# Performance work log

Measured on AMD Instinct MI355X. Metric: run time of the kernel, lower is better.

Reference implementation:

```python
import jax, jax.numpy as jnp
import numpy as np

D_MODEL = 1024
N_HEAD = 16
D_HEAD = D_MODEL // N_HEAD


def setup_inputs() -> dict:
    key = jax.random.key(0)
    ks = jax.random.split(key, 5)
    x = jax.random.normal(ks[0], (4, 2048, D_MODEL), dtype=jnp.float32)
    s = 1.0 / np.sqrt(D_MODEL)
    W_qkv = jax.random.normal(ks[1], (D_MODEL, 3 * D_MODEL), dtype=jnp.float32) * s
    b_qkv = jnp.zeros((3 * D_MODEL,), dtype=jnp.float32)
    W_out = jax.random.normal(ks[2], (D_MODEL, D_MODEL), dtype=jnp.float32) * s
    b_out = jnp.zeros((D_MODEL,), dtype=jnp.float32)
    return {"x": x, "W_qkv": W_qkv, "b_qkv": b_qkv, "W_out": W_out, "b_out": b_out}


def reference(x, W_qkv, b_qkv, W_out, b_out):
    B, T, C = x.shape
    qkv = x @ W_qkv + b_qkv                      # [B,T,3C]
    q, k, v = jnp.split(qkv, 3, axis=-1)
    def heads(t):
        return t.reshape(B, T, N_HEAD, D_HEAD).transpose(0, 2, 1, 3)  # [B,H,T,Dh]
    q, k, v = heads(q), heads(k), heads(v)
    scale = 1.0 / np.sqrt(D_HEAD)
    attn = jnp.einsum('bhqd,bhkd->bhqk', q, k) * scale  # [B,H,T,T]
    causal = jnp.tril(jnp.ones((T, T), dtype=bool))
    attn = jnp.where(causal, attn, -jnp.inf)
    attn = jax.nn.softmax(attn, axis=-1)
    out = jnp.einsum('bhqk,bhkd->bhqd', attn, v)  # [B,H,T,Dh]
    out = out.transpose(0, 2, 1, 3).reshape(B, T, C)
    return out @ W_out + b_out
```

## Files before the change

### kernel.cpp

```cpp
#include <hip/hip_runtime.h>

typedef __bf16 bf16;
typedef __bf16 bf16x4 __attribute__((ext_vector_type(4)));
typedef __bf16 bf16x8 __attribute__((ext_vector_type(8)));
typedef float f32x4 __attribute__((ext_vector_type(4)));

#define T_SEQ 2048
#define QK_LD 2048

extern "C" __device__ float __ocml_native_exp2_f32(float);

__global__ void prep_kernel(const float* __restrict__ x, bf16* __restrict__ xb,
                            const float* __restrict__ Wq, bf16* __restrict__ Wtq,
                            const float* __restrict__ Wo, bf16* __restrict__ Wto) {
    __shared__ float tile[32][33];
    const int t = threadIdx.x;
    if (blockIdx.x < 8192) {
        const int i = (blockIdx.x * 256 + t) * 4;
        const float4 f = *(const float4*)(x + i);
        bf16x4 o;
        o.x = (bf16)f.x; o.y = (bf16)f.y; o.z = (bf16)f.z; o.w = (bf16)f.w;
        *(bf16x4*)(xb + i) = o;
        return;
    }
    const int bid = blockIdx.x - 8192;
    const int xblk = bid & 127, yblk = bid >> 7;
    const bool isQ = xblk < 96;
    const float* W = isQ ? Wq : Wo;
    bf16* Wt = isQ ? Wtq : Wto;
    const int C = isQ ? 3072 : 1024;
    const int R = 1024;
    const int bx = (isQ ? xblk : (xblk - 96)) * 32;
    const int by = yblk * 32;
    const int tx = t & 31, ty = t >> 5;
#pragma unroll
    for (int i = 0; i < 32; i += 8)
        tile[ty + i][tx] = W[(size_t)(by + ty + i) * C + bx + tx];
    __syncthreads();
#pragma unroll
    for (int i = 0; i < 32; i += 8)
        Wt[(size_t)(bx + ty + i) * R + by + tx] = (bf16)tile[tx][ty + i];
}

template <bool OUT_BF16, bool SPLIT_V>
__global__ __launch_bounds__(256, 3)
void gemm_bt(const bf16* __restrict__ A, const bf16* __restrict__ Bt,
             const float* __restrict__ bias, void* __restrict__ Cout,
             bf16* __restrict__ Vtb, int M, int N, int K, int ldC) {
    __shared__ bf16 sm[16384];

    const int t = threadIdx.x;
    const int lane = t & 63, quad = lane >> 4, l16 = lane & 15;
    const int wave = t >> 6;
    const int wm = (wave >> 1) * 64;
    const int wn = (wave & 1) * 64;
    const long m0 = (long)blockIdx.y * 128;
    const long n0 = (long)blockIdx.x * 128;

    f32x4 acc[4][4] = {};

    const int sr = t >> 2, sc = t & 3;
    const int swz  = (sr * 4 + (sc ^ ((sr >> 1) & 3))) * 8;
    const int swz2 = ((sr + 64) * 4 + (sc ^ ((sr >> 1) & 3))) * 8;
    const bf16* agp = A  + (m0 + sr) * (long)K + sc * 8;
    const bf16* bgp = Bt + (n0 + sr) * (long)K + sc * 8;
    const long rowK = (long)64 * K;

    int offA[4], offB[4];
#pragma unroll
    for (int i = 0; i < 4; ++i) {
        const int row = wm + i * 16 + l16;
        offA[i] = (row * 4 + (quad ^ ((row >> 1) & 3))) * 8;
    }
#pragma unroll
    for (int j = 0; j < 4; ++j) {
        const int row = wn + j * 16 + l16;
        offB[j] = 4096 + (row * 4 + (quad ^ ((row >> 1) & 3))) * 8;
    }

    uint4 s0a0, s0a1, s0b0, s0b1;
    uint4 s1a0, s1a1, s1b0, s1b1;

    auto load0 = [&](int k) {
        s0a0 = *(const uint4*)(agp + k);        s0a1 = *(const uint4*)(agp + rowK + k);
        s0b0 = *(const uint4*)(bgp + k);        s0b1 = *(const uint4*)(bgp + rowK + k);
    };
    auto load1 = [&](int k) {
        s1a0 = *(const uint4*)(agp + k);        s1a1 = *(const uint4*)(agp + rowK + k);
        s1b0 = *(const uint4*)(bgp + k);        s1b1 = *(const uint4*)(bgp + rowK + k);
    };
    auto write0 = [&]() {
        *(uint4*)(sm + swz)         = s0a0;  *(uint4*)(sm + swz2)        = s0a1;
        *(uint4*)(sm + 4096 + swz)  = s0b0;  *(uint4*)(sm + 4096 + swz2) = s0b1;
    };
    auto write1 = [&]() {
        bf16* base = sm + 8192;
        *(uint4*)(base + swz)         = s1a0;  *(uint4*)(base + swz2)        = s1a1;
        *(uint4*)(base + 4096 + swz)  = s1b0;  *(uint4*)(base + 4096 + swz2) = s1b1;
    };
    auto compute = [&](const bf16* s) {
        bf16x8 af[4], bfr[4];
#pragma unroll
        for (int i = 0; i < 4; ++i) af[i] = *(const bf16x8*)(s + offA[i]);
#pragma unroll
        for (int j = 0; j < 4; ++j) bfr[j] = *(const bf16x8*)(s + offB[j]);
#pragma unroll
        for (int i = 0; i < 4; ++i)
#pragma unroll
            for (int j = 0; j < 4; ++j)
                acc[i][j] = __builtin_amdgcn_mfma_f32_16x16x32_bf16(bfr[j], af[i], acc[i][j], 0, 0, 0);
    };

    const int nk = K >> 5;
    load0(0);
    load1(32);
    write0();
    load0(64);
    __syncthreads();

    for (int kk = 0; kk < nk; kk += 2) {
        if (kk + 1 < nk) {
            write1();
            if (kk + 3 < nk) load1((kk + 3) * 32);
        }
        compute(sm);
        if (kk + 1 < nk) {
            __syncthreads();
            if (kk + 2 < nk) {
                write0();
                if (kk + 4 < nk) load0((kk + 4) * 32);
            }
            compute(sm + 8192);
            if (kk + 2 < nk) __syncthreads();
        }
    }

    bf16*  Cb = (bf16*)Cout;
    float* Cf = (float*)Cout;
    const bool vblock = SPLIT_V && (n0 >= 2048);
#pragma unroll
    for (int i = 0; i < 4; ++i) {
        const long gm = m0 + wm + i * 16 + l16;
#pragma unroll
        for (int j = 0; j < 4; ++j) {
            const int nloc = wn + j * 16 + quad * 4;
            const long n = n0 + nloc;
            const float4 bv = *(const float4*)(bias + n);
            float v[4];
#pragma unroll
            for (int r = 0; r < 4; ++r) v[r] = acc[i][j][r] + (&bv.x)[r];
            if (vblock) {
                const int bb = (int)(gm >> 11), tok = (int)(gm & 2047);
                const int nv = (int)(n - 2048);
                const int h = nv >> 6, d0 = nv & 63;
                bf16* dst = Vtb + ((size_t)(bb * 16 + h) * 64 + d0) * T_SEQ + tok;
#pragma unroll
                for (int r = 0; r < 4; ++r) dst[(size_t)r * T_SEQ] = (bf16)v[r];
            } else if (OUT_BF16) {
                bf16x4 o;
#pragma unroll
                for (int r = 0; r < 4; ++r) o[r] = (bf16)v[r];
                *(bf16x4*)(Cb + gm * ldC + n) = o;
            } else {
                float4 o;
#pragma unroll
                for (int r = 0; r < 4; ++r) (&o.x)[r] = v[r];
                *(float4*)(Cf + gm * ldC + n) = o;
            }
        }
    }
}

__global__ __launch_bounds__(256, 3)
void attn_kernel(const bf16* __restrict__ qk, const bf16* __restrict__ vtb,
                 bf16* __restrict__ Out) {
    const int bh = blockIdx.x;
    const int qt = 15 - (int)blockIdx.y;
    const int b = bh >> 4, h = bh & 15;
    const int t = threadIdx.x;
    const int wave = t >> 6, lane = t & 63, quad = lane >> 4, l16 = lane & 15;
    const int wq = wave * 32;
    const int q0 = qt * 128;

    __shared__ bf16 Ks[2][4096];
    __shared__ bf16 VTs[2][4096];
    __shared__ bf16 Ps[8192];

    const bf16* Qg = qk + (size_t)b * T_SEQ * QK_LD + h * 64;
    const bf16* Kg = Qg + 1024;
    const bf16* vth = vtb + (size_t)bh * 64 * T_SEQ;

    for (int c = t; c < 1024; c += 256) {
        const int row = c >> 3, kb = c & 7;
        *(uint4*)(Ps + row * 64 + (((kb ^ (row & 7)) << 3))) =
            *(const uint4*)(Qg + (size_t)(q0 + row) * QK_LD + kb * 8);
    }
    __syncthreads();
    const float qsc = 0.125f * 1.4426950408889634f;
    bf16x8 qf[2][2];
#pragma unroll
    for (int jt = 0; jt < 2; ++jt)
#pragma unroll
        for (int s = 0; s < 2; ++s) {
            const int row = wq + jt * 16 + l16;
            bf16x8 v = *(const bf16x8*)(Ps + row * 64 + (((s * 4 + quad) ^ (row & 7)) << 3));
#pragma unroll
            for (int e = 0; e < 8; ++e) v[e] = (bf16)((float)v[e] * qsc);
            qf[jt][s] = v;
        }

    const int sr = t >> 3;
    const int skb = (t & 7) ^ (sr & 7);
    const bf16* kp0 = Kg + (size_t)sr * QK_LD + skb * 8;
    const bf16* kp1 = kp0 + (size_t)32 * QK_LD;
    const bf16* vp0 = vth + (size_t)sr * T_SEQ + skb * 8;
    const bf16* vp1 = vp0 + (size_t)32 * T_SEQ;

    int offKV[4][2];
#pragma unroll
    for (int it = 0; it < 4; ++it)
#pragma unroll
        for (int s = 0; s < 2; ++s) {
            const int row = it * 16 + l16;
            offKV[it][s] = row * 64 + (((s * 4 + quad) ^ (row & 7)) << 3);
        }

    f32x4 oacc[4][2] = {};
    float lsum[2] = {0.f, 0.f};
    const int nkt = qt * 2 + 2;

    uint4 kr0 = *(const uint4*)kp0, kr1 = *(const uint4*)kp1;
    uint4 vr0 = *(const uint4*)vp0, vr1 = *(const uint4*)vp1;

    for (int kt = 0; kt < nkt; ++kt) {
        const int k0 = kt * 64;
        bf16* kb_ = Ks[kt & 1];
        bf16* vb_ = VTs[kt & 1];
        *(uint4*)(kb_ + t * 8)        = kr0;
        *(uint4*)(kb_ + 2048 + t * 8) = kr1;
        *(uint4*)(vb_ + t * 8)        = vr0;
        *(uint4*)(vb_ + 2048 + t * 8) = vr1;
        __syncthreads();

        if (kt + 1 < nkt) {
            const int kn = k0 + 64;
            kr0 = *(const uint4*)(kp0 + (size_t)kn * QK_LD);
            kr1 = *(const uint4*)(kp1 + (size_t)kn * QK_LD);
            vr0 = *(const uint4*)(vp0 + kn);
            vr1 = *(const uint4*)(vp1 + kn);
        }

        f32x4 sacc[4][2] = {};
#pragma unroll
        for (int s = 0; s < 2; ++s) {
            bf16x8 kf[4];
#pragma unroll
            for (int it = 0; it < 4; ++it)
                kf[it] = *(const bf16x8*)(kb_ + offKV[it][s]);
#pragma unroll
            for (int it = 0; it < 4; ++it)
#pragma unroll
                for (int jt = 0; jt < 2; ++jt)
                    sacc[it][jt] = __builtin_amdgcn_mfma_f32_16x16x32_bf16(kf[it], qf[jt][s], sacc[it][jt], 0, 0, 0);
        }

        const bool need_mask = (kt >= 2 * qt);
#pragma unroll
        for (int it = 0; it < 4; ++it)
#pragma unroll
            for (int jt = 0; jt < 2; ++jt) {
                const int prow = wq + jt * 16 + l16;
                bf16x4 pb;
                if (need_mask) {
                    const int qrow = q0 + prow;
                    const int kbase = k0 + it * 16 + quad * 4;
#pragma unroll
                    for (int r = 0; r < 4; ++r) {
                        const float e = __ocml_native_exp2_f32(sacc[it][jt][r]);
                        const float p = (kbase + r > qrow) ? 0.f : e;
                        lsum[jt] += p;
                        pb[r] = (bf16)p;
                    }
                } else {
#pragma unroll
                    for (int r = 0; r < 4; ++r) {
                        const float p = __ocml_native_exp2_f32(sacc[it][jt][r]);
                        lsum[jt] += p;
                        pb[r] = (bf16)p;
                    }
                }
                *(bf16x4*)(Ps + prow * 64 +
                           (((it * 2 + (quad >> 1)) ^ (prow & 7)) << 3) + ((quad & 1) << 2)) = pb;
            }

#pragma unroll
        for (int s2 = 0; s2 < 2; ++s2) {
            bf16x8 vf[4], pf[2];
#pragma unroll
            for (int it2 = 0; it2 < 4; ++it2)
                vf[it2] = *(const bf16x8*)(vb_ + offKV[it2][s2]);
#pragma unroll
            for (int jt = 0; jt < 2; ++jt) {
                const int prow = wq + jt * 16 + l16;
                pf[jt] = *(const bf16x8*)(Ps + prow * 64 + (((s2 * 4 + quad) ^ (prow & 7)) << 3));
            }
#pragma unroll
            for (int it2 = 0; it2 < 4; ++it2)
#pragma unroll
                for (int jt = 0; jt < 2; ++jt)
                    oacc[it2][jt] = __builtin_amdgcn_mfma_f32_16x16x32_bf16(vf[it2], pf[jt], oacc[it2][jt], 0, 0, 0);
        }
    }

    float inv[2];
#pragma unroll
    for (int jt = 0; jt < 2; ++jt) {
        float l = lsum[jt];
        l += __shfl_xor(l, 16);
        l += __shfl_xor(l, 32);
        inv[jt] = 1.0f / l;
    }
#pragma unroll
    for (int it2 = 0; it2 < 4; ++it2)
#pragma unroll
        for (int jt = 0; jt < 2; ++jt) {
            bf16x4 ob;
#pragma unroll
            for (int r = 0; r < 4; ++r) ob[r] = (bf16)(oacc[it2][jt][r] * inv[jt]);
            const int qrow = q0 + wq + jt * 16 + l16;
            const int dcol = h * 64 + it2 * 16 + quad * 4;
            *(bf16x4*)&Out[(size_t)(b * T_SEQ + qrow) * 1024 + dcol] = ob;
        }
}

extern "C" void kernel_launch(void* const* d_in, const int* in_sizes, int n_in,
                              void* d_out, int out_size, void* d_ws, size_t ws_size,
                              hipStream_t stream) {
    const float* x     = (const float*)d_in[0];
    const float* W_qkv = (const float*)d_in[1];
    const float* b_qkv = (const float*)d_in[2];
    const float* W_out = (const float*)d_in[3];
    const float* b_out = (const float*)d_in[4];
    float* out = (float*)d_out;

    char* ws = (char*)d_ws;
    bf16* xb   = (bf16*)ws; ws += (size_t)8192 * 1024 * 2;
    bf16* wtq  = (bf16*)ws; ws += (size_t)3072 * 1024 * 2;
    bf16* wto  = (bf16*)ws; ws += (size_t)1024 * 1024 * 2;
    bf16* qkb  = (bf16*)ws; ws += (size_t)8192 * 2048 * 2;
    bf16* vtb  = (bf16*)ws; ws += (size_t)64 * 64 * 2048 * 2;
    bf16* aout = (bf16*)ws; ws += (size_t)8192 * 1024 * 2;

    prep_kernel<<<8192 + 4096, 256, 0, stream>>>(x, xb, W_qkv, wtq, W_out, wto);

    gemm_bt<true, true><<<dim3(24, 64), 256, 0, stream>>>(
        xb, wtq, b_qkv, (void*)qkb, vtb, 8192, 3072, 1024, 2048);
    attn_kernel<<<dim3(64, 16), 256, 0, stream>>>(qkb, vtb, aout);
    gemm_bt<false, false><<<dim3(8, 64), 256, 0, stream>>>(
        aout, wto, b_out, (void*)out, nullptr, 8192, 1024, 1024, 1024);
}
```

Baseline: 247.0 us.

## Add 256x256-tile GEMM with direct global-to-LDS loads for QKV projection

```diff
diff --git a/kernel.cpp b/kernel.cpp
--- a/kernel.cpp
+++ b/kernel.cpp
@@ -9,6 +9,11 @@
 #define QK_LD 2048
 
 extern "C" __device__ float __ocml_native_exp2_f32(float);
+
+#define GLOAD16(gp, lp)                                                        \
+  __builtin_amdgcn_global_load_lds(                                            \
+      (const __attribute__((address_space(1))) unsigned int*)(gp),             \
+      (__attribute__((address_space(3))) unsigned int*)(lp), 16, 0, 0)
 
 __global__ void prep_kernel(const float* __restrict__ x, bf16* __restrict__ xb,
                             const float* __restrict__ Wq, bf16* __restrict__ Wtq,
@@ -40,6 +45,146 @@
 #pragma unroll
     for (int i = 0; i < 32; i += 8)
         Wt[(size_t)(bx + ty + i) * R + by + tx] = (bf16)tile[tx][ty + i];
+}
+
+template <bool OUT_BF16, bool SPLIT_V>
+__global__ __launch_bounds__(512, 2)
+void gemm256(const bf16* __restrict__ A, const bf16* __restrict__ Bt,
+             const float* __restrict__ bias, void* __restrict__ Cout,
+             bf16* __restrict__ Vtb, int M, int N, int K, int ldC) {
+    __shared__ bf16 sm[65536];
+
+    const int t = threadIdx.x;
+    const int lane = t & 63, quad = lane >> 4, l16 = lane & 15;
+    const int wv = t >> 6;
+    const int wm = (wv >> 2) * 64;
+    const int wn = (wv & 3) * 32;
+    const long m0 = (long)blockIdx.y * 256;
+    const long n0 = (long)blockIdx.x * 256;
+    (void)M; (void)N;
+
+    f32x4 acc[2][2][4][2] = {};
+
+    const int srow = t >> 3;
+    const int scol = ((t & 7) ^ ((t >> 3) & 7)) * 8;
+    const bf16* agp = A  + (m0 + srow) * (long)K + scol;
+    const bf16* bgp = Bt + (n0 + srow) * (long)K + scol;
+    const long rowK64  = (long)64 * K;
+    const long rowK128 = (long)128 * K;
+    bf16* ldst = sm + wv * 512;
+
+    auto stage = [&](int buf, int oper, int half, int kt) {
+        const bf16* src = (oper ? bgp : agp) + (long)kt * 64 + (half ? rowK128 : 0);
+        bf16* dst = ldst + buf * 32768 + oper * 16384 + half * 8192;
+        GLOAD16(src, dst);
+        GLOAD16(src + rowK64, dst + 4096);
+    };
+
+    int offA[4][2], offB[2][2];
+#pragma unroll
+    for (int i = 0; i < 4; ++i)
+#pragma unroll
+        for (int ks = 0; ks < 2; ++ks) {
+            const int r = wm + i * 16 + l16;
+            offA[i][ks] = r * 64 + (((ks * 4 + quad) ^ (r & 7)) << 3);
+        }
+#pragma unroll
+    for (int j = 0; j < 2; ++j)
+#pragma unroll
+        for (int ks = 0; ks < 2; ++ks) {
+            const int r = wn + j * 16 + l16;
+            offB[j][ks] = r * 64 + (((ks * 4 + quad) ^ (r & 7)) << 3);
+        }
+
+#define PHASE(BUF, MQ, NQ, DOSTAGE, SOP, SHF, SKT, WAITSTR) do {               \
+    const bf16* sb_  = sm + (BUF) * 32768;                                     \
+    const bf16* sa_  = sb_ + (MQ) * 8192;                                      \
+    const bf16* sbb_ = sb_ + 16384 + (NQ) * 8192;                              \
+    bf16x8 af_[2][4], bv_[2][2];                                               \
+    _Pragma("unroll") for (int ks = 0; ks < 2; ++ks) {                         \
+        _Pragma("unroll") for (int i = 0; i < 4; ++i)                          \
+            af_[ks][i] = *(const bf16x8*)(sa_ + offA[i][ks]);                  \
+        _Pragma("unroll") for (int j = 0; j < 2; ++j)                          \
+            bv_[ks][j] = *(const bf16x8*)(sbb_ + offB[j][ks]);                 \
+    }                                                                          \
+    if (DOSTAGE) stage((BUF) ^ 1, SOP, SHF, SKT);                              \
+    __builtin_amdgcn_s_barrier();                                              \
+    __builtin_amdgcn_s_setprio(1);                                             \
+    _Pragma("unroll") for (int ks = 0; ks < 2; ++ks)                           \
+        _Pragma("unroll") for (int i = 0; i < 4; ++i)                          \
+            _Pragma("unroll") for (int j = 0; j < 2; ++j)                      \
+                acc[MQ][NQ][i][j] = __builtin_amdgcn_mfma_f32_16x16x32_bf16(   \
+                    bv_[ks][j], af_[ks][i], acc[MQ][NQ][i][j], 0, 0, 0);       \
+    __builtin_amdgcn_s_setprio(0);                                             \
+    asm volatile(WAITSTR ::: "memory");                                        \
+    __builtin_amdgcn_s_barrier();                                              \
+    __builtin_amdgcn_sched_barrier(0);                                         \
+} while (0)
+
+    const int nkt = K >> 6;
+
+    stage(0, 0, 0, 0);
+    stage(0, 1, 0, 0);
+    stage(0, 0, 1, 0);
+    stage(0, 1, 1, 0);
+    asm volatile("s_waitcnt vmcnt(4)" ::: "memory");
+    __builtin_amdgcn_s_barrier();
+    __builtin_amdgcn_sched_barrier(0);
+
+    for (int kt = 0; kt < nkt - 1; ++kt) {
+        const int buf = kt & 1;
+        const int kn = kt + 1;
+        PHASE(buf, 0, 0, true, 0, 0, kn, "s_waitcnt vmcnt(4)");
+        PHASE(buf, 1, 0, true, 1, 0, kn, "s_waitcnt vmcnt(4)");
+        PHASE(buf, 0, 1, true, 0, 1, kn, "");
+        PHASE(buf, 1, 1, true, 1, 1, kn, "s_waitcnt vmcnt(4)");
+    }
+    {
+        const int buf = (nkt - 1) & 1;
+        PHASE(buf, 0, 0, false, 0, 0, 0, "s_waitcnt vmcnt(2)");
+        PHASE(buf, 1, 0, false, 0, 0, 0, "s_waitcnt vmcnt(0)");
+        PHASE(buf, 0, 1, false, 0, 0, 0, "");
+        PHASE(buf, 1, 1, false, 0, 0, 0, "");
+    }
+#undef PHASE
+
+    bf16*  Cb = (bf16*)Cout;
+    float* Cf = (float*)Cout;
+    const bool vblock = SPLIT_V && (n0 >= 2048);
+#pragma unroll
+    for (int mq = 0; mq < 2; ++mq)
+#pragma unroll
+    for (int i = 0; i < 4; ++i) {
+        const long gm = m0 + mq * 128 + wm + i * 16 + l16;
+#pragma unroll
+        for (int nq = 0; nq < 2; ++nq)
+#pragma unroll
+        for (int j = 0; j < 2; ++j) {
+            const long n = n0 + nq * 128 + wn + j * 16 + quad * 4;
+            const float4 bv = *(const float4*)(bias + n);
+            float v[4];
+#pragma unroll
+            for (int r = 0; r < 4; ++r) v[r] = acc[mq][nq][i][j][r] + (&bv.x)[r];
+            if (vblock) {
+                const int bb = (int)(gm >> 11), tok = (int)(gm & 2047);
+                const int nv = (int)(n - 2048);
+                const int h = nv >> 6, d0 = nv & 63;
+                bf16* dst = Vtb + ((size_t)(bb * 16 + h) * 64 + d0) * T_SEQ + tok;
+#pragma unroll
+                for (int r = 0; r < 4; ++r) dst[(size_t)r * T_SEQ] = (bf16)v[r];
+            } else if (OUT_BF16) {
+                bf16x4 o;
+#pragma unroll
+                for (int r = 0; r < 4; ++r) o[r] = (bf16)v[r];
+                *(bf16x4*)(Cb + gm * ldC + n) = o;
+            } else {
+                float4 o;
+#pragma unroll
+                for (int r = 0; r < 4; ++r) (&o.x)[r] = v[r];
+                *(float4*)(Cf + gm * ldC + n) = o;
+            }
+        }
+    }
 }
 
 template <bool OUT_BF16, bool SPLIT_V>
@@ -353,7 +498,7 @@
 
     prep_kernel<<<8192 + 4096, 256, 0, stream>>>(x, xb, W_qkv, wtq, W_out, wto);
 
-    gemm_bt<true, true><<<dim3(24, 64), 256, 0, stream>>>(
+    gemm256<true, true><<<dim3(12, 32), 512, 0, stream>>>(
         xb, wtq, b_qkv, (void*)qkb, vtb, 8192, 3072, 1024, 2048);
     attn_kernel<<<dim3(64, 16), 256, 0, stream>>>(qkb, vtb, aout);
     gemm_bt<false, false><<<dim3(8, 64), 256, 0, stream>>>(
```

Measured after the change: 250.7 us. Within noise of the previous version (+1.5%).

## Load GEMM tiles directly into LDS with global_load_lds and deeper K tile

Applied to the files above, without the earlier changes.

```diff
diff --git a/kernel.cpp b/kernel.cpp
--- a/kernel.cpp
+++ b/kernel.cpp
@@ -9,6 +9,11 @@
 #define QK_LD 2048
 
 extern "C" __device__ float __ocml_native_exp2_f32(float);
+
+#define GLOAD16(gp, lp)                                                        \
+  __builtin_amdgcn_global_load_lds(                                            \
+      (const __attribute__((address_space(1))) unsigned int*)(gp),             \
+      (__attribute__((address_space(3))) unsigned int*)(lp), 16, 0, 0)
 
 __global__ void prep_kernel(const float* __restrict__ x, bf16* __restrict__ xb,
                             const float* __restrict__ Wq, bf16* __restrict__ Wtq,
@@ -43,11 +48,11 @@
 }
 
 template <bool OUT_BF16, bool SPLIT_V>
-__global__ __launch_bounds__(256, 3)
-void gemm_bt(const bf16* __restrict__ A, const bf16* __restrict__ Bt,
+__global__ __launch_bounds__(256, 2)
+void gemm128(const bf16* __restrict__ A, const bf16* __restrict__ Bt,
              const float* __restrict__ bias, void* __restrict__ Cout,
              bf16* __restrict__ Vtb, int M, int N, int K, int ldC) {
-    __shared__ bf16 sm[16384];
+    __shared__ bf16 sm[32768];
 
     const int t = threadIdx.x;
     const int lane = t & 63, quad = lane >> 4, l16 = lane & 15;
@@ -56,82 +61,72 @@
     const int wn = (wave & 1) * 64;
     const long m0 = (long)blockIdx.y * 128;
     const long n0 = (long)blockIdx.x * 128;
+    (void)M; (void)N;
 
     f32x4 acc[4][4] = {};
 
-    const int sr = t >> 2, sc = t & 3;
-    const int swz  = (sr * 4 + (sc ^ ((sr >> 1) & 3))) * 8;
-    const int swz2 = ((sr + 64) * 4 + (sc ^ ((sr >> 1) & 3))) * 8;
-    const bf16* agp = A  + (m0 + sr) * (long)K + sc * 8;
-    const bf16* bgp = Bt + (n0 + sr) * (long)K + sc * 8;
-    const long rowK = (long)64 * K;
-
-    int offA[4], offB[4];
-#pragma unroll
-    for (int i = 0; i < 4; ++i) {
-        const int row = wm + i * 16 + l16;
-        offA[i] = (row * 4 + (quad ^ ((row >> 1) & 3))) * 8;
-    }
-#pragma unroll
-    for (int j = 0; j < 4; ++j) {
-        const int row = wn + j * 16 + l16;
-        offB[j] = 4096 + (row * 4 + (quad ^ ((row >> 1) & 3))) * 8;
-    }
-
-    uint4 s0a0, s0a1, s0b0, s0b1;
-    uint4 s1a0, s1a1, s1b0, s1b1;
-
-    auto load0 = [&](int k) {
-        s0a0 = *(const uint4*)(agp + k);        s0a1 = *(const uint4*)(agp + rowK + k);
-        s0b0 = *(const uint4*)(bgp + k);        s0b1 = *(const uint4*)(bgp + rowK + k);
+    const int srow = t >> 3;
+    const int scol = ((t & 7) ^ ((t >> 3) & 7)) * 8;
+    const bf16* agp = A  + (m0 + srow) * (long)K + scol;
+    const bf16* bgp = Bt + (n0 + srow) * (long)K + scol;
+    const long rowK32 = (long)32 * K;
+
+    auto stage = [&](int buf, int kt) {
+        bf16* d = sm + buf * 16384 + t * 8;
+        const bf16* a = agp + (long)kt * 64;
+        const bf16* b = bgp + (long)kt * 64;
+        GLOAD16(a,               d);
+        GLOAD16(a +     rowK32,  d + 2048);
+        GLOAD16(a + 2 * rowK32,  d + 4096);
+        GLOAD16(a + 3 * rowK32,  d + 6144);
+        GLOAD16(b,               d + 8192);
+        GLOAD16(b +     rowK32,  d + 10240);
+        GLOAD16(b + 2 * rowK32,  d + 12288);
+        GLOAD16(b + 3 * rowK32,  d + 14336);
     };
-    auto load1 = [&](int k) {
-        s1a0 = *(const uint4*)(agp + k);        s1a1 = *(const uint4*)(agp + rowK + k);
-        s1b0 = *(const uint4*)(bgp + k);        s1b1 = *(const uint4*)(bgp + rowK + k);
-    };
-    auto write0 = [&]() {
-        *(uint4*)(sm + swz)         = s0a0;  *(uint4*)(sm + swz2)        = s0a1;
-        *(uint4*)(sm + 4096 + swz)  = s0b0;  *(uint4*)(sm + 4096 + swz2) = s0b1;
-    };
-    auto write1 = [&]() {
-        bf16* base = sm + 8192;
-        *(uint4*)(base + swz)         = s1a0;  *(uint4*)(base + swz2)        = s1a1;
-        *(uint4*)(base + 4096 + swz)  = s1b0;  *(uint4*)(base + 4096 + swz2) = s1b1;
-    };
-    auto compute = [&](const bf16* s) {
-        bf16x8 af[4], bfr[4];
-#pragma unroll
-        for (int i = 0; i < 4; ++i) af[i] = *(const bf16x8*)(s + offA[i]);
-#pragma unroll
-        for (int j = 0; j < 4; ++j) bfr[j] = *(const bf16x8*)(s + offB[j]);
-#pragma unroll
-        for (int i = 0; i < 4; ++i)
-#pragma unroll
-            for (int j = 0; j < 4; ++j)
-                acc[i][j] = __builtin_amdgcn_mfma_f32_16x16x32_bf16(bfr[j], af[i], acc[i][j], 0, 0, 0);
-    };
-
-    const int nk = K >> 5;
-    load0(0);
-    load1(32);
-    write0();
-    load0(64);
-    __syncthreads();
-
-    for (int kk = 0; kk < nk; kk += 2) {
-        if (kk + 1 < nk) {
-            write1();
-            if (kk + 3 < nk) load1((kk + 3) * 32);
-        }
-        compute(sm);
-        if (kk + 1 < nk) {
-            __syncthreads();
-            if (kk + 2 < nk) {
-                write0();
-                if (kk + 4 < nk) load0((kk + 4) * 32);
+
+    int offA[4][2], offB[4][2];
+#pragma unroll
+    for (int i = 0; i < 4; ++i)
+#pragma unroll
+        for (int ks = 0; ks < 2; ++ks) {
+            const int rA = wm + i * 16 + l16;
+            offA[i][ks] = rA * 64 + (((ks * 4 + quad) ^ (rA & 7)) << 3);
+            const int rB = wn + i * 16 + l16;
+            offB[i][ks] = 8192 + rB * 64 + (((ks * 4 + quad) ^ (rB & 7)) << 3);
+        }
+
+    const int nkt = K >> 6;
+
+    stage(0, 0);
+    asm volatile("s_waitcnt vmcnt(0)" ::: "memory");
+    __builtin_amdgcn_s_barrier();
+    __builtin_amdgcn_sched_barrier(0);
+
+    for (int kt = 0; kt < nkt; ++kt) {
+        const int buf = kt & 1;
+        if (kt + 1 < nkt) stage(buf ^ 1, kt + 1);
+        const bf16* base_ = sm + buf * 16384;
+        bf16x8 fA[2][4], fB[2][4];
+#pragma unroll
+        for (int ks = 0; ks < 2; ++ks)
+#pragma unroll
+            for (int i = 0; i < 4; ++i) {
+                fA[ks][i] = *(const bf16x8*)(base_ + offA[i][ks]);
+                fB[ks][i] = *(const bf16x8*)(base_ + offB[i][ks]);
             }
-            compute(sm + 8192);
-            if (kk + 2 < nk) __syncthreads();
+#pragma unroll
+        for (int ks = 0; ks < 2; ++ks)
+#pragma unroll
+            for (int i = 0; i < 4; ++i)
+#pragma unroll
+                for (int j = 0; j < 4; ++j)
+                    acc[i][j] = __builtin_amdgcn_mfma_f32_16x16x32_bf16(
+                        fB[ks][j], fA[ks][i], acc[i][j], 0, 0, 0);
+        if (kt + 1 < nkt) {
+            asm volatile("s_waitcnt vmcnt(0)" ::: "memory");
+            __builtin_amdgcn_s_barrier();
+            __builtin_amdgcn_sched_barrier(0);
         }
     }
 
@@ -353,9 +348,9 @@
 
     prep_kernel<<<8192 + 4096, 256, 0, stream>>>(x, xb, W_qkv, wtq, W_out, wto);
 
-    gemm_bt<true, true><<<dim3(24, 64), 256, 0, stream>>>(
+    gemm128<true, true><<<dim3(24, 64), 256, 0, stream>>>(
         xb, wtq, b_qkv, (void*)qkb, vtb, 8192, 3072, 1024, 2048);
     attn_kernel<<<dim3(64, 16), 256, 0, stream>>>(qkb, vtb, aout);
-    gemm_bt<false, false><<<dim3(8, 64), 256, 0, stream>>>(
+    gemm128<false, false><<<dim3(8, 64), 256, 0, stream>>>(
         aout, wto, b_out, (void*)out, nullptr, 8192, 1024, 1024, 1024);
 }
```

After: 232.4 us (median of 2 runs). 5.9% less time.
